# Performance work log

Measured on AMD Instinct MI355X. Metric: run time of the kernel, lower is better.

The kernel has to match this reference:

```python
import jax, jax.numpy as jnp
import numpy as np
from jax import lax

H = 8          # num_heads
STATE = 16     # SSM state_dim
EPS = 1e-5


def layer_norm(x, g, b):
    mu = jnp.mean(x, axis=-1, keepdims=True)
    var = jnp.mean((x - mu) ** 2, axis=-1, keepdims=True)
    return (x - mu) / jnp.sqrt(var + EPS) * g + b


def linear(x, w, b):
    # torch nn.Linear convention: w [out,in]
    return x @ w.T + b


def cross_attn(q_in, kv_in, qw, qb, kw, kb, vw, vb, ow, ob, g, beta):
    B, Lq, D = q_in.shape
    Lk = kv_in.shape[1]
    hd = D // H
    Q = linear(q_in, qw, qb).reshape(B, Lq, H, hd).transpose(0, 2, 1, 3)
    K = linear(kv_in, kw, kb).reshape(B, Lk, H, hd).transpose(0, 2, 1, 3)
    V = linear(kv_in, vw, vb).reshape(B, Lk, H, hd).transpose(0, 2, 1, 3)
    scores = jnp.einsum('bhqd,bhkd->bhqk', Q, K) / (hd ** 0.5)
    w = jax.nn.softmax(scores, axis=-1)
    out = jnp.einsum('bhqk,bhkd->bhqd', w, V)
    out = out.transpose(0, 2, 1, 3).reshape(B, Lq, D)
    out = linear(out, ow, ob)
    out = layer_norm(out + q_in, g, beta)
    return out, w


def ssm(x, in_w, in_b, A, Bm, C, gw, gb, ow, ob):
    B, L, D = x.shape
    xp = linear(x, in_w, in_b)                      # [B,L,2D]
    x_in = xp[..., D:]                              # second chunk
    gate = jax.nn.sigmoid(linear(x, gw, gb))
    x_in = x_in * gate
    def step(h, xt):
        h = h @ A.T + xt @ Bm.T                     # [B,STATE]
        return h, h @ C.T                           # y [B,D]
    h0 = jnp.zeros((B, STATE), dtype=x.dtype)
    _, ys = lax.scan(step, h0, x_in.transpose(1, 0, 2))
    ys = ys.transpose(1, 0, 2)
    return linear(ys, ow, ob)


def mamba_block(x, p, i):
    y = ssm(layer_norm(x, p['m_ln1_g'][i], p['m_ln1_b'][i]),
            p['m_in_w'][i], p['m_in_b'][i], p['m_A'][i], p['m_B'][i], p['m_C'][i],
            p['m_gate_w'][i], p['m_gate_b'][i], p['m_sout_w'][i], p['m_sout_b'][i])
    x = x + y
    h = layer_norm(x, p['m_ln2_g'][i], p['m_ln2_b'][i])
    h = linear(h, p['m_f1_w'][i], p['m_f1_b'][i])
    h = jax.nn.gelu(h, approximate=False)
    h = linear(h, p['m_f2_w'][i], p['m_f2_b'][i])
    return x + h


def setup_inputs() -> dict:
    key = jax.random.key(0)
    ks = iter(jax.random.split(key, 64))
    B, L, D, BD, VD = 1024, 32, 256, 128, 256
    nB = 6
    def rn(shape, s=0.02):
        return jax.random.normal(next(ks), shape, dtype=jnp.float32) * s
    inp = {
        'ble_features': jax.random.normal(next(ks), (B, L, BD), dtype=jnp.float32),
        'visual_features': jax.random.normal(next(ks), (B, L, VD), dtype=jnp.float32),
        # modality projections
        'bp_w': rn((D, BD)), 'bp_b': jnp.zeros(D), 'bp_emb': rn((D,)),
        'bp_g': jnp.ones(D), 'bp_beta': jnp.zeros(D),
        'vp_w': rn((D, VD)), 'vp_b': jnp.zeros(D), 'vp_emb': rn((D,)),
        'vp_g': jnp.ones(D), 'vp_beta': jnp.zeros(D),
        # two cross-attentions stacked on axis 0: [0]=ble->vis, [1]=vis->ble
        'a_qw': rn((2, D, D)), 'a_qb': jnp.zeros((2, D)),
        'a_kw': rn((2, D, D)), 'a_kb': jnp.zeros((2, D)),
        'a_vw': rn((2, D, D)), 'a_vb': jnp.zeros((2, D)),
        'a_ow': rn((2, D, D)), 'a_ob': jnp.zeros((2, D)),
        'a_g': jnp.ones((2, D)), 'a_beta': jnp.zeros((2, D)),
        # 6 mamba blocks stacked on axis 0
        'm_ln1_g': jnp.ones((nB, D)), 'm_ln1_b': jnp.zeros((nB, D)),
        'm_in_w': rn((nB, 2 * D, D)), 'm_in_b': jnp.zeros((nB, 2 * D)),
        'm_A': rn((nB, STATE, STATE)), 'm_B': rn((nB, STATE, D)), 'm_C': rn((nB, D, STATE)),
        'm_gate_w': rn((nB, D, D)), 'm_gate_b': jnp.zeros((nB, D)),
        'm_sout_w': rn((nB, D, D)), 'm_sout_b': jnp.zeros((nB, D)),
        'm_ln2_g': jnp.ones((nB, D)), 'm_ln2_b': jnp.zeros((nB, D)),
        'm_f1_w': rn((nB, 4 * D, D)), 'm_f1_b': jnp.zeros((nB, 4 * D)),
        'm_f2_w': rn((nB, D, 4 * D)), 'm_f2_b': jnp.zeros((nB, D)),
        # final projection
        'fin_g': jnp.ones(D), 'fin_beta': jnp.zeros(D),
        'fin_w': rn((D, D)), 'fin_b': jnp.zeros(D),
    }
    return inp


def reference(ble_features, visual_features,
              bp_w, bp_b, bp_emb, bp_g, bp_beta,
              vp_w, vp_b, vp_emb, vp_g, vp_beta,
              a_qw, a_qb, a_kw, a_kb, a_vw, a_vb, a_ow, a_ob, a_g, a_beta,
              m_ln1_g, m_ln1_b, m_in_w, m_in_b, m_A, m_B, m_C,
              m_gate_w, m_gate_b, m_sout_w, m_sout_b,
              m_ln2_g, m_ln2_b, m_f1_w, m_f1_b, m_f2_w, m_f2_b,
              fin_g, fin_beta, fin_w, fin_b):
    ble = layer_norm(linear(ble_features, bp_w, bp_b) + bp_emb, bp_g, bp_beta)
    vis = layer_norm(linear(visual_features, vp_w, vp_b) + vp_emb, vp_g, vp_beta)
    # seq_len == target_length -> align_sequences is identity
    ble_att, w_b2v = cross_attn(ble, vis, a_qw[0], a_qb[0], a_kw[0], a_kb[0],
                                a_vw[0], a_vb[0], a_ow[0], a_ob[0], a_g[0], a_beta[0])
    vis_att, w_v2b = cross_attn(vis, ble, a_qw[1], a_qb[1], a_kw[1], a_kb[1],
                                a_vw[1], a_vb[1], a_ow[1], a_ob[1], a_g[1], a_beta[1])
    fused = ble_att + vis_att
    p = dict(m_ln1_g=m_ln1_g, m_ln1_b=m_ln1_b, m_in_w=m_in_w, m_in_b=m_in_b,
             m_A=m_A, m_B=m_B, m_C=m_C, m_gate_w=m_gate_w, m_gate_b=m_gate_b,
             m_sout_w=m_sout_w, m_sout_b=m_sout_b, m_ln2_g=m_ln2_g, m_ln2_b=m_ln2_b,
             m_f1_w=m_f1_w, m_f1_b=m_f1_b, m_f2_w=m_f2_w, m_f2_b=m_f2_b)
    for i in range(m_A.shape[0]):
        fused = mamba_block(fused, p, i)
    g = jnp.mean(fused, axis=1)
    g = layer_norm(g, fin_g, fin_beta)
    g = jax.nn.gelu(linear(g, fin_w, fin_b), approximate=False)
    wb = jnp.mean(w_b2v, axis=(1, 2, 3))
    wv = jnp.mean(w_v2b, axis=(1, 2, 3))
    tot = wb + wv + 1e-6
    return (g, wb / tot, wv / tot)
```

## Files before the change

kernel.cpp:

```cpp
#include <hip/hip_runtime.h>
#include <hip/hip_bf16.h>
#include <math.h>

static constexpr int Bsz  = 1024;
static constexpr int Lseq = 32;
static constexpr int Dm   = 256;
static constexpr int NROW = Bsz * Lseq;

typedef __attribute__((ext_vector_type(8))) short bf16x8;
typedef __attribute__((ext_vector_type(4))) float f32x4;

__device__ __forceinline__ float sigm_f(float x) {
    return 1.0f / (1.0f + __expf(-x));
}
__device__ __forceinline__ float gelu_f(float x) {
    const float u = x * (0.7978845608028654f + 0.0356774081f * x * x);
    return x * sigm_f(2.0f * u);
}
__device__ __forceinline__ float b2f(ushort u) {
    union { float f; uint v; } t; t.v = ((uint)u) << 16; return t.f;
}
__device__ __forceinline__ ushort f2b(float f) {
    union { float f; uint v; } t; t.f = f;
    const uint lsb = (t.v >> 16) & 1u;
    t.v += 0x7fffu + lsb;
    return (ushort)(t.v >> 16);
}

#define GLDS(gp, lp) __builtin_amdgcn_global_load_lds( \
    (const __attribute__((address_space(1))) void*)(gp), \
    (__attribute__((address_space(3))) void*)(lp), 16, 0, 0)

template<int ACT, bool OUTBF, int OMAP, int DUAL>
__global__ __launch_bounds__(256)
void mgemm(const ushort* __restrict__ X, const ushort* __restrict__ W,
           const ushort* __restrict__ W2,
           const float* __restrict__ b1, const float* __restrict__ b2,
           float* __restrict__ Cf, ushort* __restrict__ Cb,
           ushort* __restrict__ Cb2, int K, int M)
{
    __shared__ ushort As[4096];
    __shared__ ushort Bs[4096];
    __shared__ ushort Bs2[DUAL ? 4096 : 8];
    __shared__ ushort Rx[DUAL ? 4096 : 8192];
    const int tid = threadIdx.x;
    const int w = tid >> 6, l = tid & 63;

    int f = blockIdx.y * gridDim.x + blockIdx.x;
    const int nwg = gridDim.x * gridDim.y;
    if ((nwg & 7) == 0) f = (f & 7) * (nwg >> 3) + (f >> 3);
    const int n0 = (f / gridDim.x) << 7;
    const int m0 = (f % gridDim.x) << 7;

    const int ric  = l >> 2;
    const int slot = l & 3;
    const int rL0 = (w << 4) + ric;
    const int rL1 = rL0 + 64;
    const int sw0 = slot ^ ((rL0 >> 1) & 3);
    const int sw1 = slot ^ ((rL1 >> 1) & 3);
    const ushort* gA0 = X + (size_t)(n0 + rL0) * K + (sw0 << 3);
    const ushort* gA1 = X + (size_t)(n0 + rL1) * K + (sw1 << 3);
    const ushort* gB0 = W + (size_t)(m0 + rL0) * K + (sw0 << 3);
    const ushort* gB1 = W + (size_t)(m0 + rL1) * K + (sw1 << 3);
    const ushort* gC0 = nullptr; const ushort* gC1 = nullptr;
    if constexpr (DUAL) {
        gC0 = W2 + (size_t)(m0 + rL0) * K + (sw0 << 3);
        gC1 = W2 + (size_t)(m0 + rL1) * K + (sw1 << 3);
    }
    ushort* lA0 = As + ((size_t)w << 9);
    ushort* lA1 = As + ((size_t)(w + 4) << 9);
    ushort* lB0 = Bs + ((size_t)w << 9);
    ushort* lB1 = Bs + ((size_t)(w + 4) << 9);
    ushort* lC0 = Bs2 + ((size_t)w << 9);
    ushort* lC1 = Bs2 + ((size_t)(w + 4) << 9);

    const int wr = (w >> 1) & 1, wc = w & 1;
    const int cl = l & 15, kg = l >> 4;
    int aoff[4], boff[4];
    #pragma unroll
    for (int m = 0; m < 4; ++m) {
        const int r = wr * 64 + m * 16 + cl;
        aoff[m] = r * 32 + ((kg ^ ((r >> 1) & 3)) << 3);
    }
    #pragma unroll
    for (int n = 0; n < 4; ++n) {
        const int r = wc * 64 + n * 16 + cl;
        boff[n] = r * 32 + ((kg ^ ((r >> 1) & 3)) << 3);
    }

    f32x4 acc[4][4];
    f32x4 acc2[DUAL ? 4 : 1][DUAL ? 4 : 1];
    #pragma unroll
    for (int m = 0; m < 4; ++m)
        #pragma unroll
        for (int n = 0; n < 4; ++n) {
            acc[m][n] = (f32x4){0.f, 0.f, 0.f, 0.f};
            if constexpr (DUAL) acc2[m][n] = (f32x4){0.f, 0.f, 0.f, 0.f};
        }

    for (int kc = 0; kc < K; kc += 32) {
        GLDS(gA0, lA0); GLDS(gA1, lA1);
        GLDS(gB0, lB0); GLDS(gB1, lB1);
        gA0 += 32; gA1 += 32; gB0 += 32; gB1 += 32;
        if constexpr (DUAL) {
            GLDS(gC0, lC0); GLDS(gC1, lC1);
            gC0 += 32; gC1 += 32;
        }
        __syncthreads();
        bf16x8 av[4], bv[4];
        #pragma unroll
        for (int m = 0; m < 4; ++m) av[m] = *(const bf16x8*)(As + aoff[m]);
        #pragma unroll
        for (int n = 0; n < 4; ++n) bv[n] = *(const bf16x8*)(Bs + boff[n]);
        #pragma unroll
        for (int m = 0; m < 4; ++m)
            #pragma unroll
            for (int n = 0; n < 4; ++n)
                acc[m][n] = __builtin_amdgcn_mfma_f32_16x16x32_bf16(
                    av[m], bv[n], acc[m][n], 0, 0, 0);
        if constexpr (DUAL) {
            bf16x8 cv[4];
            #pragma unroll
            for (int n = 0; n < 4; ++n) cv[n] = *(const bf16x8*)(Bs2 + boff[n]);
            #pragma unroll
            for (int m = 0; m < 4; ++m)
                #pragma unroll
                for (int n = 0; n < 4; ++n)
                    acc2[m][n] = __builtin_amdgcn_mfma_f32_16x16x32_bf16(
                        av[m], cv[n], acc2[m][n], 0, 0, 0);
        }
        __syncthreads();
    }

    const int colb = m0 + wc * 64 + cl;
    const int rowb = n0 + wr * 64 + (kg << 2);
    float biasA[4], biasB[4];
    #pragma unroll
    for (int n = 0; n < 4; ++n) {
        biasA[n] = (b1 != nullptr) ? b1[colb + n * 16] : 0.0f;
        if constexpr (DUAL) biasB[n] = b2[colb + n * 16];
    }

    if constexpr (OUTBF || DUAL != 0) {
        ushort* Rw;
        if constexpr (DUAL) Rw = (w == 0) ? As : (w == 1) ? Bs : (w == 2) ? Bs2 : Rx;
        else                Rw = (w == 0) ? As : (w == 1) ? Bs : Rx + ((w - 2) << 12);
        const int rr = l >> 3, rc8 = (l & 7) << 3;
        const int nout = (DUAL == 2) ? 2 : 1;
        for (int which = 0; which < nout; ++which) {
            #pragma unroll
            for (int m = 0; m < 4; ++m)
                #pragma unroll
                for (int j = 0; j < 4; ++j) {
                    const int lrow = m * 16 + (kg << 2) + j;
                    #pragma unroll
                    for (int n = 0; n < 4; ++n) {
                        float v;
                        if (which == 0) {
                            v = acc[m][n][j] + biasA[n];
                            if constexpr (DUAL == 1)
                                v = sigm_f(v) * (acc2[m][n][j] + biasB[n]);
                            else if (ACT == 1) v = sigm_f(v);
                            else if (ACT == 2) v = gelu_f(v);
                        } else {
                            v = acc2[m][n][j] + biasB[n];
                        }
                        const int lcol = (n << 4) + cl;
                        Rw[lrow * 64 + (lcol ^ (((lrow >> 1) & 7) << 3))] = f2b(v);
                    }
                }
            ushort* dst = (which == 0) ? Cb : Cb2;
            #pragma unroll
            for (int p = 0; p < 8; ++p) {
                const int lrow = (p << 3) + rr;
                const bf16x8 v8 = *(const bf16x8*)(
                    Rw + lrow * 64 + (rc8 ^ (((lrow >> 1) & 7) << 3)));
                const size_t grow = (size_t)(n0 + wr * 64 + lrow);
                const int gcol = m0 + wc * 64 + rc8;
                size_t idx;
                if (OMAP == 1) idx = grow * 1024 + ((size_t)(gcol >> 4) << 5) + (gcol & 15);
                else           idx = grow * (size_t)M + gcol;
                *(bf16x8*)(dst + idx) = v8;
            }
        }
    } else {
        #pragma unroll
        for (int m = 0; m < 4; ++m)
            #pragma unroll
            for (int j = 0; j < 4; ++j) {
                const size_t row = (size_t)(rowb + m * 16 + j);
                #pragma unroll
                for (int n = 0; n < 4; ++n) {
                    float v = acc[m][n][j] + biasA[n];
                    if (ACT == 1) v = sigm_f(v);
                    else if (ACT == 2) v = gelu_f(v);
                    Cf[row * (size_t)M + colb + n * 16] = v;
                }
            }
    }
}

template<bool ADD_E, bool ACC_F, bool WRV, int LNOUT, bool HASB2>
__global__ __launch_bounds__(256)
void growln_k(const ushort* __restrict__ X, const ushort* __restrict__ W,
              const float* __restrict__ b1, const float* __restrict__ b2,
              const float* __restrict__ E, const float* __restrict__ g,
              const float* __restrict__ bt, float* __restrict__ Fres,
              ushort* __restrict__ Yb, int K)
{
    __shared__ ushort As[64 * 32];
    __shared__ ushort Bs[256 * 32];
    const int tid = threadIdx.x;
    const int w = tid >> 6, l = tid & 63;
    const int n0 = blockIdx.x << 6;

    const int ric = l >> 2, slot = l & 3;
    const int rA  = (w << 4) + ric;
    const int swA = slot ^ ((rA >> 1) & 3);
    const ushort* gA = X + (size_t)(n0 + rA) * K + (swA << 3);
    ushort* lA = As + (w << 9);
    const int rB0 = (w << 4) + ric;
    const int rB1 = rB0 + 64, rB2 = rB0 + 128, rB3 = rB0 + 192;
    const ushort* gB0 = W + (size_t)rB0 * K + ((slot ^ ((rB0 >> 1) & 3)) << 3);
    const ushort* gB1 = W + (size_t)rB1 * K + ((slot ^ ((rB1 >> 1) & 3)) << 3);
    const ushort* gB2 = W + (size_t)rB2 * K + ((slot ^ ((rB2 >> 1) & 3)) << 3);
    const ushort* gB3 = W + (size_t)rB3 * K + ((slot ^ ((rB3 >> 1) & 3)) << 3);
    ushort* lB0 = Bs + (w << 9);
    ushort* lB1 = Bs + ((4 + w) << 9);
    ushort* lB2 = Bs + ((8 + w) << 9);
    ushort* lB3 = Bs + ((12 + w) << 9);

    const int cl = l & 15, kg = l >> 4;
    const int ar = (w << 4) + cl;
    const int aoff = ar * 32 + ((kg ^ ((ar >> 1) & 3)) << 3);
    int boff[16];
    #pragma unroll
    for (int n = 0; n < 16; ++n) {
        const int br = n * 16 + cl;
        boff[n] = br * 32 + ((kg ^ ((br >> 1) & 3)) << 3);
    }

    f32x4 acc[16];
    #pragma unroll
    for (int n = 0; n < 16; ++n) acc[n] = (f32x4){0.f, 0.f, 0.f, 0.f};

    for (int kc = 0; kc < K; kc += 32) {
        GLDS(gA, lA);   gA  += 32;
        GLDS(gB0, lB0); gB0 += 32;
        GLDS(gB1, lB1); gB1 += 32;
        GLDS(gB2, lB2); gB2 += 32;
        GLDS(gB3, lB3); gB3 += 32;
        __syncthreads();
        const bf16x8 av = *(const bf16x8*)(As + aoff);
        #pragma unroll
        for (int n = 0; n < 16; ++n) {
            const bf16x8 bv = *(const bf16x8*)(Bs + boff[n]);
            acc[n] = __builtin_amdgcn_mfma_f32_16x16x32_bf16(av, bv, acc[n], 0, 0, 0);
        }
        __syncthreads();
    }

    float bA[16];
    #pragma unroll
    for (int n = 0; n < 16; ++n) {
        float v = (b1 != nullptr) ? b1[n * 16 + cl] : 0.0f;
        if (HASB2) v += b2[n * 16 + cl];
        bA[n] = v;
    }
    float gg[16], bb[16];
    if (LNOUT > 0) {
        #pragma unroll
        for (int n = 0; n < 16; ++n) { gg[n] = g[n * 16 + cl]; bb[n] = bt[n * 16 + cl]; }
    }

    #pragma unroll
    for (int j = 0; j < 4; ++j) {
        const int r = n0 + (w << 4) + (kg << 2) + j;
        const size_t rb = (size_t)r << 8;
        float v[16];
        float s = 0.0f;
        #pragma unroll
        for (int n = 0; n < 16; ++n) {
            float x = acc[n][j] + bA[n];
            if (ADD_E) x += E[rb + n * 16 + cl];
            if (ACC_F) x += Fres[rb + n * 16 + cl];
            v[n] = x; s += x;
        }
        if (WRV) {
            #pragma unroll
            for (int n = 0; n < 16; ++n) Fres[rb + n * 16 + cl] = v[n];
        }
        if (LNOUT > 0) {
            #pragma unroll
            for (int o = 1; o < 16; o <<= 1) s += __shfl_xor(s, o);
            const float mu = s * (1.0f / 256.0f);
            float q = 0.0f;
            #pragma unroll
            for (int n = 0; n < 16; ++n) { const float d = v[n] - mu; q += d * d; }
            #pragma unroll
            for (int o = 1; o < 16; o <<= 1) q += __shfl_xor(q, o);
            const float rstd = rsqrtf(q * (1.0f / 256.0f) + 1e-5f);
            #pragma unroll
            for (int n = 0; n < 16; ++n) {
                const float y = (v[n] - mu) * rstd * gg[n] + bb[n];
                const size_t idx = rb + n * 16 + cl;
                if (LNOUT & 1) Yb[idx] = f2b(y);
                if (LNOUT == 2 || LNOUT == 3) Fres[idx] = y;
                if (LNOUT == 4) Fres[idx] += y;
            }
        }
    }
}

__global__ __launch_bounds__(256)
void ln_k(const float* __restrict__ X, const float* __restrict__ g,
          const float* __restrict__ bt, ushort* __restrict__ Yb)
{
    const int lane = threadIdx.x & 63;
    const int row  = (blockIdx.x << 2) + (threadIdx.x >> 6);
    const size_t base = (size_t)row * Dm + (lane << 2);
    float4 v = *reinterpret_cast<const float4*>(&X[base]);
    float s = v.x + v.y + v.z + v.w;
    #pragma unroll
    for (int o = 1; o < 64; o <<= 1) s += __shfl_xor(s, o);
    const float mu = s * (1.0f / 256.0f);
    const float d0 = v.x - mu, d1 = v.y - mu, d2 = v.z - mu, d3 = v.w - mu;
    float q = d0*d0 + d1*d1 + d2*d2 + d3*d3;
    #pragma unroll
    for (int o = 1; o < 64; o <<= 1) q += __shfl_xor(q, o);
    const float rstd = rsqrtf(q * (1.0f / 256.0f) + 1e-5f);
    const int c = lane << 2;
    const float4 gg = *reinterpret_cast<const float4*>(&g[c]);
    const float4 bb = *reinterpret_cast<const float4*>(&bt[c]);
    ushort4 ub;
    ub.x = f2b(d0*rstd*gg.x + bb.x); ub.y = f2b(d1*rstd*gg.y + bb.y);
    ub.z = f2b(d2*rstd*gg.z + bb.z); ub.w = f2b(d3*rstd*gg.w + bb.w);
    *reinterpret_cast<ushort4*>(&Yb[base]) = ub;
}

__global__ __launch_bounds__(256)
void attn_k(const ushort* __restrict__ Q, const ushort* __restrict__ K,
            const ushort* __restrict__ V, ushort* __restrict__ O)
{
    __shared__ float Qs[32][33], Ks[32][33], Vs[32][33], Ss[32][33];
    const int bh = blockIdx.x;
    const int b = bh >> 3, h = bh & 7;
    const int tid = threadIdx.x;
    const int r  = tid >> 3;
    const int c4 = (tid & 7) << 2;
    const size_t base = ((size_t)b * Lseq + r) * Dm + h * 32 + c4;
    {
        const ushort4 q = *reinterpret_cast<const ushort4*>(&Q[base]);
        Qs[r][c4+0]=b2f(q.x); Qs[r][c4+1]=b2f(q.y); Qs[r][c4+2]=b2f(q.z); Qs[r][c4+3]=b2f(q.w);
        const ushort4 k = *reinterpret_cast<const ushort4*>(&K[base]);
        Ks[r][c4+0]=b2f(k.x); Ks[r][c4+1]=b2f(k.y); Ks[r][c4+2]=b2f(k.z); Ks[r][c4+3]=b2f(k.w);
        const ushort4 v = *reinterpret_cast<const ushort4*>(&V[base]);
        Vs[r][c4+0]=b2f(v.x); Vs[r][c4+1]=b2f(v.y); Vs[r][c4+2]=b2f(v.z); Vs[r][c4+3]=b2f(v.w);
    }
    __syncthreads();
    float sc[4] = {0.f, 0.f, 0.f, 0.f};
    #pragma unroll
    for (int d = 0; d < 32; ++d) {
        const float qv = Qs[r][d];
        #pragma unroll
        for (int j = 0; j < 4; ++j) sc[j] = fmaf(qv, Ks[c4+j][d], sc[j]);
    }
    #pragma unroll
    for (int j = 0; j < 4; ++j) sc[j] *= 0.17677669529663687f;
    float mx = fmaxf(fmaxf(sc[0], sc[1]), fmaxf(sc[2], sc[3]));
    #pragma unroll
    for (int o = 1; o < 8; o <<= 1) mx = fmaxf(mx, __shfl_xor(mx, o));
    float sum = 0.f;
    #pragma unroll
    for (int j = 0; j < 4; ++j) { sc[j] = __expf(sc[j] - mx); sum += sc[j]; }
    #pragma unroll
    for (int o = 1; o < 8; o <<= 1) sum += __shfl_xor(sum, o);
    const float inv = 1.0f / sum;
    #pragma unroll
    for (int j = 0; j < 4; ++j) Ss[r][c4+j] = sc[j] * inv;
    __syncthreads();
    float o4[4] = {0.f, 0.f, 0.f, 0.f};
    #pragma unroll
    for (int k = 0; k < 32; ++k) {
        const float wv = Ss[r][k];
        #pragma unroll
        for (int j = 0; j < 4; ++j) o4[j] = fmaf(wv, Vs[k][c4+j], o4[j]);
    }
    ushort4 ob; ob.x=f2b(o4[0]); ob.y=f2b(o4[1]); ob.z=f2b(o4[2]); ob.w=f2b(o4[3]);
    *reinterpret_cast<ushort4*>(&O[base]) = ob;
}

__global__ __launch_bounds__(256)
void xb_gemm(const ushort* __restrict__ X, const ushort* __restrict__ Bw,
             ushort* __restrict__ XB)
{
    __shared__ ushort As[128 * 32];
    __shared__ ushort Bsf[16 * 256];
    const int tid = threadIdx.x;
    const int w = tid >> 6, l = tid & 63;
    const int n0 = blockIdx.x << 7;
    #pragma unroll
    for (int rep = 0; rep < 2; ++rep) {
        const int u = (rep << 8) + tid;
        const int r = u >> 5;
        const int c8 = (u & 31) << 3;
        const int di = (r * 256 + c8) ^ ((r & 7) << 3);
        *(bf16x8*)(Bsf + di) = *(const bf16x8*)(Bw + r * 256 + c8);
    }
    const int ric = l >> 2, slot = l & 3;
    const int rL0 = (w << 4) + ric, rL1 = rL0 + 64;
    const int sw0 = slot ^ ((rL0 >> 1) & 3), sw1 = slot ^ ((rL1 >> 1) & 3);
    const ushort* gA0 = X + (size_t)(n0 + rL0) * 256 + (sw0 << 3);
    const ushort* gA1 = X + (size_t)(n0 + rL1) * 256 + (sw1 << 3);
    ushort* lA0 = As + (w << 9);
    ushort* lA1 = As + ((w + 4) << 9);
    const int cl = l & 15, kg = l >> 4;
    int aoff[2];
    #pragma unroll
    for (int m = 0; m < 2; ++m) {
        const int r = w * 32 + m * 16 + cl;
        aoff[m] = r * 32 + ((kg ^ ((r >> 1) & 3)) << 3);
    }
    f32x4 acc[2] = {(f32x4){0.f,0.f,0.f,0.f}, (f32x4){0.f,0.f,0.f,0.f}};
    for (int kc = 0; kc < 256; kc += 32) {
        GLDS(gA0, lA0); GLDS(gA1, lA1);
        gA0 += 32; gA1 += 32;
        __syncthreads();
        const bf16x8 av0 = *(const bf16x8*)(As + aoff[0]);
        const bf16x8 av1 = *(const bf16x8*)(As + aoff[1]);
        const int bidx = (cl * 256 + kc + (kg << 3)) ^ ((cl & 7) << 3);
        const bf16x8 bv = *(const bf16x8*)(Bsf + bidx);
        acc[0] = __builtin_amdgcn_mfma_f32_16x16x32_bf16(av0, bv, acc[0], 0, 0, 0);
        acc[1] = __builtin_amdgcn_mfma_f32_16x16x32_bf16(av1, bv, acc[1], 0, 0, 0);
        __syncthreads();
    }
    #pragma unroll
    for (int m = 0; m < 2; ++m)
        #pragma unroll
        for (int j = 0; j < 4; ++j) {
            const int row = n0 + w * 32 + m * 16 + (kg << 2) + j;
            XB[(size_t)row * 16 + cl] = f2b(acc[m][j]);
        }
}

__global__ __launch_bounds__(256)
void powT_k(const float* __restrict__ A_all, ushort* __restrict__ T_all)
{
    __shared__ float P[2][16][16];
    __shared__ float Asm[16][16];
    const int layer = blockIdx.x;
    const float* A = A_all + layer * 256;
    ushort* T = T_all + (size_t)layer * 262144;
    const int tid = threadIdx.x;
    const int i = tid >> 4, j = tid & 15;
    Asm[i][j] = A[tid];
    const bf16x8 z = {0,0,0,0,0,0,0,0};
    for (int u = tid; u < 32768; u += 256)
        *(bf16x8*)(T + (size_t)u * 8) = z;
    P[0][i][j] = (i == j) ? 1.0f : 0.0f;
    __syncthreads();
    for (int k = 0; k < 32; ++k) {
        const float pv = P[k & 1][i][j];
        const ushort pb = f2b(pv);
        for (int tau = 0; tau + k < 32; ++tau)
            T[(size_t)((tau + k) * 16 + i) * 512 + tau * 16 + j] = pb;
        float acc = 0.0f;
        #pragma unroll
        for (int l2 = 0; l2 < 16; ++l2) acc = fmaf(P[k & 1][i][l2], Asm[l2][j], acc);
        P[(k & 1) ^ 1][i][j] = acc;
        __syncthreads();
    }
}

__global__ __launch_bounds__(256)
void zeroH_k(ushort* __restrict__ Hp)
{
    const int i = blockIdx.x * 256 + threadIdx.x;
    const bf16x8 z = {0,0,0,0,0,0,0,0};
    *(bf16x8*)(Hp + (size_t)i * 8) = z;
}

__global__ __launch_bounds__(256)
void wsc_k(const float* __restrict__ sw, const float* __restrict__ Cc,
           ushort* __restrict__ Wp)
{
    const int i = blockIdx.x >> 4;
    const int m = ((blockIdx.x & 15) << 4) + (threadIdx.x >> 4);
    const int s = threadIdx.x & 15;
    const float* swr = sw + ((size_t)i << 16) + (m << 8);
    const float* cc  = Cc + ((size_t)i << 12) + s;
    float acc = 0.0f;
    #pragma unroll 8
    for (int d = 0; d < 256; ++d) acc = fmaf(swr[d], cc[d << 4], acc);
    ushort* o = Wp + ((size_t)i << 13) + (m << 5);
    o[s] = f2b(acc);
    o[s + 16] = 0;
}

__global__ __launch_bounds__(256)
void meanL_k(const float* __restrict__ X, float* __restrict__ G)
{
    const int idx = blockIdx.x * 256 + threadIdx.x;
    const int b = idx >> 8, d = idx & 255;
    const float* xp = X + (size_t)b * (Lseq * Dm) + d;
    float s = 0.0f;
    #pragma unroll
    for (int t = 0; t < Lseq; ++t) s += xp[t << 8];
    G[idx] = s * (1.0f / 32.0f);
}

__global__ __launch_bounds__(256)
void fillw_k(float* __restrict__ out)
{
    const int i = blockIdx.x * 256 + threadIdx.x;
    const float wm = 1.0f / 32.0f;
    out[i] = wm / (wm + wm + 1e-6f);
}

__global__ __launch_bounds__(256)
void cast_k(const float* __restrict__ src, ushort* __restrict__ dst, int n4)
{
    const int i = blockIdx.x * 256 + threadIdx.x;
    if (i < n4) {
        const float4 v = reinterpret_cast<const float4*>(src)[i];
        ushort4 o; o.x = f2b(v.x); o.y = f2b(v.y); o.z = f2b(v.z); o.w = f2b(v.w);
        reinterpret_cast<ushort4*>(dst)[i] = o;
    }
}

__global__ __launch_bounds__(256)
void cast_inw_k(const float* __restrict__ src, ushort* __restrict__ dst)
{
    const int i = blockIdx.x * 256 + threadIdx.x;
    const int blk = i >> 14, rem = i & 16383;
    const float4 v = reinterpret_cast<const float4*>(
        src + (size_t)blk * 131072 + 65536)[rem];
    ushort4 o; o.x = f2b(v.x); o.y = f2b(v.y); o.z = f2b(v.z); o.w = f2b(v.w);
    reinterpret_cast<ushort4*>(dst)[i] = o;
}

extern "C" void kernel_launch(void* const* d_in, const int* in_sizes, int n_in,
                              void* d_out, int out_size, void* d_ws, size_t ws_size,
                              hipStream_t stream)
{
    const float* ble_f   = (const float*)d_in[0];
    const float* vis_f   = (const float*)d_in[1];
    const float* bp_w    = (const float*)d_in[2];
    const float* bp_b    = (const float*)d_in[3];
    const float* bp_emb  = (const float*)d_in[4];
    const float* bp_g    = (const float*)d_in[5];
    const float* bp_beta = (const float*)d_in[6];
    const float* vp_w    = (const float*)d_in[7];
    const float* vp_b    = (const float*)d_in[8];
    const float* vp_emb  = (const float*)d_in[9];
    const float* vp_g    = (const float*)d_in[10];
    const float* vp_beta = (const float*)d_in[11];
    const float* a_qw    = (const float*)d_in[12];
    const float* a_qb    = (const float*)d_in[13];
    const float* a_kw    = (const float*)d_in[14];
    const float* a_kb    = (const float*)d_in[15];
    const float* a_vw    = (const float*)d_in[16];
    const float* a_vb    = (const float*)d_in[17];
    const float* a_ow    = (const float*)d_in[18];
    const float* a_ob    = (const float*)d_in[19];
    const float* a_g     = (const float*)d_in[20];
    const float* a_beta  = (const float*)d_in[21];
    const float* m_ln1_g = (const float*)d_in[22];
    const float* m_ln1_b = (const float*)d_in[23];
    const float* m_in_w  = (const float*)d_in[24];
    const float* m_in_b  = (const float*)d_in[25];
    const float* m_A     = (const float*)d_in[26];
    const float* m_B     = (const float*)d_in[27];
    const float* m_C     = (const float*)d_in[28];
    const float* m_gw    = (const float*)d_in[29];
    const float* m_gb    = (const float*)d_in[30];
    const float* m_sw    = (const float*)d_in[31];
    const float* m_sb    = (const float*)d_in[32];
    const float* m_ln2_g = (const float*)d_in[33];
    const float* m_ln2_b = (const float*)d_in[34];
    const float* m_f1w   = (const float*)d_in[35];
    const float* m_f1b   = (const float*)d_in[36];
    const float* m_f2w   = (const float*)d_in[37];
    const float* m_f2b   = (const float*)d_in[38];
    const float* fin_g   = (const float*)d_in[39];
    const float* fin_beta= (const float*)d_in[40];
    const float* fin_w   = (const float*)d_in[41];
    const float* fin_b   = (const float*)d_in[42];

    float* out = (float*)d_out;
    float* ws  = (float*)d_ws;
    const size_t NDf = (size_t)NROW * Dm;

    float* F_res = ws;
    float* F0 = ws + 1 * NDf;
    float* F1 = ws + 2 * NDf;
    float* F2 = ws + 3 * NDf;
    ushort* S0 = (ushort*)(ws + 4 * NDf);
    ushort* S1 = S0 + NDf;
    ushort* S2 = S1 + NDf;
    ushort* S3 = S2 + NDf;
    ushort* S4 = S3 + NDf;
    ushort* Wa = S4 + NDf;
    ushort* W_bp  = Wa;
    ushort* W_vp  = W_bp + 32768;
    ushort* W_q   = W_vp + 65536;
    ushort* W_k   = W_q + 131072;
    ushort* W_v   = W_k + 131072;
    ushort* W_o   = W_v + 131072;
    ushort* W_g   = W_o + 131072;
    ushort* W_in  = W_g + 393216;
    ushort* W_f1  = W_in + 393216;
    ushort* W_f2  = W_f1 + 1572864;
    ushort* W_fin = W_f2 + 1572864;
    ushort* W_sc  = W_fin + 65536;
    ushort* Hpad  = W_sc + 49152;
    ushort* B_ble = (ushort*)F2;
    ushort* B_vis = B_ble + (size_t)NROW * 128;
    ushort* T_all = (ushort*)F2;
    ushort* W_bm  = T_all + 1572864;
    ushort* XBuf  = W_bm + 24576;

    const dim3 blk(256);
    auto cgrid = [](int n4) { return dim3((n4 + 255) / 256); };

    cast_k<<<cgrid(1048576), blk, 0, stream>>>(ble_f, B_ble, 1048576);
    cast_k<<<cgrid(2097152), blk, 0, stream>>>(vis_f, B_vis, 2097152);
    cast_k<<<cgrid(8192),   blk, 0, stream>>>(bp_w, W_bp, 8192);
    cast_k<<<cgrid(16384),  blk, 0, stream>>>(vp_w, W_vp, 16384);
    cast_k<<<cgrid(32768),  blk, 0, stream>>>(a_qw, W_q, 32768);
    cast_k<<<cgrid(32768),  blk, 0, stream>>>(a_kw, W_k, 32768);
    cast_k<<<cgrid(32768),  blk, 0, stream>>>(a_vw, W_v, 32768);
    cast_k<<<cgrid(32768),  blk, 0, stream>>>(a_ow, W_o, 32768);
    cast_k<<<cgrid(98304),  blk, 0, stream>>>(m_gw, W_g, 98304);
    cast_k<<<cgrid(393216), blk, 0, stream>>>(m_f1w, W_f1, 393216);
    cast_k<<<cgrid(393216), blk, 0, stream>>>(m_f2w, W_f2, 393216);
    cast_k<<<cgrid(16384),  blk, 0, stream>>>(fin_w, W_fin, 16384);
    cast_inw_k<<<cgrid(98304), blk, 0, stream>>>(m_in_w, W_in);
    wsc_k<<<96, blk, 0, stream>>>(m_sw, m_C, W_sc);

    auto gg = [](int M, int N) { return dim3(M / 128, N / 128); };
    const dim3 gRow(NROW / 64);

    growln_k<false,false,false,3,true><<<gRow, blk, 0, stream>>>(
        B_ble, W_bp, bp_b, bp_emb, nullptr, bp_g, bp_beta, F0, S0, 128);
    growln_k<false,false,false,3,true><<<gRow, blk, 0, stream>>>(
        B_vis, W_vp, vp_b, vp_emb, nullptr, vp_g, vp_beta, F1, S1, 256);

    for (int a = 0; a < 2; ++a) {
        const ushort* qin_b = (a == 0) ? S0 : S1;
        const ushort* kin_b = (a == 0) ? S1 : S0;
        const float*  qin_f = (a == 0) ? F0 : F1;
        const size_t wo = (size_t)a * 65536;
        const size_t bo = (size_t)a * 256;
        mgemm<0,true,0,0><<<gg(256, NROW), blk, 0, stream>>>(
            qin_b, W_q + wo, nullptr, a_qb + bo, nullptr, nullptr, S4, nullptr, 256, 256);
        mgemm<0,true,0,2><<<gg(256, NROW), blk, 0, stream>>>(
            kin_b, W_k + wo, W_v + wo, a_kb + bo, a_vb + bo, nullptr, S2, S3, 256, 256);
        attn_k<<<Bsz * 8, blk, 0, stream>>>(S4, S2, S3, S4);
        if (a == 0)
            growln_k<true,false,false,2,false><<<gRow, blk, 0, stream>>>(
                S4, W_o + wo, a_ob + bo, nullptr, qin_f, a_g + bo, a_beta + bo, F_res, nullptr, 256);
        else
            growln_k<true,false,false,4,false><<<gRow, blk, 0, stream>>>(
                S4, W_o + wo, a_ob + bo, nullptr, qin_f, a_g + bo, a_beta + bo, F_res, nullptr, 256);
    }

    powT_k<<<6, blk, 0, stream>>>(m_A, T_all);
    cast_k<<<cgrid(6144), blk, 0, stream>>>(m_B, W_bm, 6144);
    zeroH_k<<<512, blk, 0, stream>>>(Hpad);

    ln_k<<<NROW/4, blk, 0, stream>>>(F_res, m_ln1_g, m_ln1_b, S0);

    for (int i = 0; i < 6; ++i) {
        mgemm<0,true,0,1><<<gg(256, NROW), blk, 0, stream>>>(
            S0, W_g + (size_t)i*65536, W_in + (size_t)i*65536,
            m_gb + i*256, m_in_b + (size_t)i*512 + 256, nullptr, S2, nullptr, 256, 256);
        xb_gemm<<<NROW/128, blk, 0, stream>>>(S2, W_bm + (size_t)i*4096, XBuf);
        mgemm<0,true,1,0><<<gg(512, 1024), blk, 0, stream>>>(
            XBuf, T_all + (size_t)i*262144, nullptr, nullptr, nullptr, nullptr, Hpad, nullptr, 512, 512);
        growln_k<false,true,true,1,false><<<gRow, blk, 0, stream>>>(
            Hpad, W_sc + (size_t)i*8192, m_sb + i*256, nullptr, nullptr,
            m_ln2_g + i*256, m_ln2_b + i*256, F_res, S0, 32);
        mgemm<2,true,0,0><<<gg(1024, NROW), blk, 0, stream>>>(
            S0, W_f1 + (size_t)i*262144, nullptr, m_f1b + i*1024, nullptr, nullptr, S1, nullptr, 256, 1024);
        if (i < 5)
            growln_k<false,true,true,1,false><<<gRow, blk, 0, stream>>>(
                S1, W_f2 + (size_t)i*262144, m_f2b + i*256, nullptr, nullptr,
                m_ln1_g + (i+1)*256, m_ln1_b + (i+1)*256, F_res, S0, 1024);
        else
            growln_k<false,true,true,0,false><<<gRow, blk, 0, stream>>>(
                S1, W_f2 + (size_t)i*262144, m_f2b + i*256, nullptr, nullptr,
                nullptr, nullptr, F_res, nullptr, 1024);
    }

    meanL_k<<<(Bsz * Dm) / 256, blk, 0, stream>>>(F_res, F0);
    ln_k<<<Bsz/4, blk, 0, stream>>>(F0, fin_g, fin_beta, S1);
    mgemm<2,false,0,0><<<gg(256, Bsz), blk, 0, stream>>>(
        S1, W_fin, nullptr, fin_b, nullptr, out, nullptr, nullptr, 256, 256);
    fillw_k<<<8, blk, 0, stream>>>(out + (size_t)Bsz * Dm);
}
```

Measured before the change: 1.306 ms.

## Split growln row tile across 2x2 warp grid with shared-memory LayerNorm reduction

The fused GEMM+LayerNorm kernel now handles 32 rows per block instead of 64. The four waves form a 2x2 grid, each covering 16 rows by 128 columns, so accumulators drop from 16 to 8 MFMA tiles per wave. Row mean and variance partials from the two column halves are combined through shared memory with extra barriers. The aim is to cut register pressure and double the block count for better occupancy and load balance. The cost is reloading the full W tile for every 32 rows, which doubles weight traffic, plus two extra syncs.

After: 1.293 ms. No clear change (-1.0%).

```diff
diff --git a/kernel.cpp b/kernel.cpp
--- a/kernel.cpp
+++ b/kernel.cpp
@@ -208,102 +208,123 @@
               const float* __restrict__ bt, float* __restrict__ Fres,
               ushort* __restrict__ Yb, int K)
 {
-    __shared__ ushort As[64 * 32];
+    __shared__ ushort As[32 * 32];
     __shared__ ushort Bs[256 * 32];
+    __shared__ float sred[32][2];
+    __shared__ float qred[32][2];
     const int tid = threadIdx.x;
     const int w = tid >> 6, l = tid & 63;
-    const int n0 = blockIdx.x << 6;
+    const int n0 = blockIdx.x << 5;
+    const int rowg = w >> 1, colg = w & 1;
 
     const int ric = l >> 2, slot = l & 3;
-    const int rA  = (w << 4) + ric;
-    const int swA = slot ^ ((rA >> 1) & 3);
-    const ushort* gA = X + (size_t)(n0 + rA) * K + (swA << 3);
-    ushort* lA = As + (w << 9);
-    const int rB0 = (w << 4) + ric;
-    const int rB1 = rB0 + 64, rB2 = rB0 + 128, rB3 = rB0 + 192;
-    const ushort* gB0 = W + (size_t)rB0 * K + ((slot ^ ((rB0 >> 1) & 3)) << 3);
-    const ushort* gB1 = W + (size_t)rB1 * K + ((slot ^ ((rB1 >> 1) & 3)) << 3);
-    const ushort* gB2 = W + (size_t)rB2 * K + ((slot ^ ((rB2 >> 1) & 3)) << 3);
-    const ushort* gB3 = W + (size_t)rB3 * K + ((slot ^ ((rB3 >> 1) & 3)) << 3);
-    ushort* lB0 = Bs + (w << 9);
-    ushort* lB1 = Bs + ((4 + w) << 9);
-    ushort* lB2 = Bs + ((8 + w) << 9);
-    ushort* lB3 = Bs + ((12 + w) << 9);
+    const ushort* gB[4]; ushort* lB[4];
+    #pragma unroll
+    for (int c = 0; c < 4; ++c) {
+        const int rB = ((w << 2) + c) * 16 + ric;
+        gB[c] = W + (size_t)rB * K + ((slot ^ ((rB >> 1) & 3)) << 3);
+        lB[c] = Bs + (((w << 2) + c) << 9);
+    }
+    const ushort* gA = nullptr; ushort* lA = nullptr;
+    if (w < 2) {
+        const int rA = (w << 4) + ric;
+        gA = X + (size_t)(n0 + rA) * K + ((slot ^ ((rA >> 1) & 3)) << 3);
+        lA = As + (w << 9);
+    }
 
     const int cl = l & 15, kg = l >> 4;
-    const int ar = (w << 4) + cl;
+    const int ar = rowg * 16 + cl;
     const int aoff = ar * 32 + ((kg ^ ((ar >> 1) & 3)) << 3);
-    int boff[16];
-    #pragma unroll
-    for (int n = 0; n < 16; ++n) {
-        const int br = n * 16 + cl;
+    int boff[8];
+    #pragma unroll
+    for (int n = 0; n < 8; ++n) {
+        const int br = colg * 128 + n * 16 + cl;
         boff[n] = br * 32 + ((kg ^ ((br >> 1) & 3)) << 3);
     }
 
-    f32x4 acc[16];
-    #pragma unroll
-    for (int n = 0; n < 16; ++n) acc[n] = (f32x4){0.f, 0.f, 0.f, 0.f};
+    f32x4 acc[8];
+    #pragma unroll
+    for (int n = 0; n < 8; ++n) acc[n] = (f32x4){0.f, 0.f, 0.f, 0.f};
 
     for (int kc = 0; kc < K; kc += 32) {
-        GLDS(gA, lA);   gA  += 32;
-        GLDS(gB0, lB0); gB0 += 32;
-        GLDS(gB1, lB1); gB1 += 32;
-        GLDS(gB2, lB2); gB2 += 32;
-        GLDS(gB3, lB3); gB3 += 32;
+        #pragma unroll
+        for (int c = 0; c < 4; ++c) { GLDS(gB[c], lB[c]); gB[c] += 32; }
+        if (w < 2) { GLDS(gA, lA); gA += 32; }
         __syncthreads();
         const bf16x8 av = *(const bf16x8*)(As + aoff);
         #pragma unroll
-        for (int n = 0; n < 16; ++n) {
+        for (int n = 0; n < 8; ++n) {
             const bf16x8 bv = *(const bf16x8*)(Bs + boff[n]);
             acc[n] = __builtin_amdgcn_mfma_f32_16x16x32_bf16(av, bv, acc[n], 0, 0, 0);
         }
         __syncthreads();
     }
 
-    float bA[16];
-    #pragma unroll
-    for (int n = 0; n < 16; ++n) {
-        float v = (b1 != nullptr) ? b1[n * 16 + cl] : 0.0f;
-        if (HASB2) v += b2[n * 16 + cl];
+    float bA[8];
+    #pragma unroll
+    for (int n = 0; n < 8; ++n) {
+        const int col = colg * 128 + n * 16 + cl;
+        float v = (b1 != nullptr) ? b1[col] : 0.0f;
+        if (HASB2) v += b2[col];
         bA[n] = v;
     }
-    float gg[16], bb[16];
+    float gg[8], bb[8];
     if (LNOUT > 0) {
         #pragma unroll
-        for (int n = 0; n < 16; ++n) { gg[n] = g[n * 16 + cl]; bb[n] = bt[n * 16 + cl]; }
+        for (int n = 0; n < 8; ++n) {
+            const int col = colg * 128 + n * 16 + cl;
+            gg[n] = g[col]; bb[n] = bt[col];
+        }
     }
 
     #pragma unroll
     for (int j = 0; j < 4; ++j) {
-        const int r = n0 + (w << 4) + (kg << 2) + j;
-        const size_t rb = (size_t)r << 8;
-        float v[16];
+        const int lrow = rowg * 16 + (kg << 2) + j;
+        const size_t rb = (size_t)(n0 + lrow) << 8;
         float s = 0.0f;
         #pragma unroll
-        for (int n = 0; n < 16; ++n) {
+        for (int n = 0; n < 8; ++n) {
+            const size_t idx = rb + colg * 128 + n * 16 + cl;
             float x = acc[n][j] + bA[n];
-            if (ADD_E) x += E[rb + n * 16 + cl];
-            if (ACC_F) x += Fres[rb + n * 16 + cl];
-            v[n] = x; s += x;
+            if (ADD_E) x += E[idx];
+            if (ACC_F) x += Fres[idx];
+            acc[n][j] = x; s += x;
         }
         if (WRV) {
             #pragma unroll
-            for (int n = 0; n < 16; ++n) Fres[rb + n * 16 + cl] = v[n];
+            for (int n = 0; n < 8; ++n)
+                Fres[rb + colg * 128 + n * 16 + cl] = acc[n][j];
         }
         if (LNOUT > 0) {
             #pragma unroll
             for (int o = 1; o < 16; o <<= 1) s += __shfl_xor(s, o);
-            const float mu = s * (1.0f / 256.0f);
+            if (cl == 0) sred[lrow][colg] = s;
+        }
+    }
+    if (LNOUT > 0) {
+        __syncthreads();
+        float mu[4];
+        #pragma unroll
+        for (int j = 0; j < 4; ++j) {
+            const int lrow = rowg * 16 + (kg << 2) + j;
+            mu[j] = (sred[lrow][0] + sred[lrow][1]) * (1.0f / 256.0f);
             float q = 0.0f;
             #pragma unroll
-            for (int n = 0; n < 16; ++n) { const float d = v[n] - mu; q += d * d; }
+            for (int n = 0; n < 8; ++n) { const float d = acc[n][j] - mu[j]; q += d * d; }
             #pragma unroll
             for (int o = 1; o < 16; o <<= 1) q += __shfl_xor(q, o);
-            const float rstd = rsqrtf(q * (1.0f / 256.0f) + 1e-5f);
-            #pragma unroll
-            for (int n = 0; n < 16; ++n) {
-                const float y = (v[n] - mu) * rstd * gg[n] + bb[n];
-                const size_t idx = rb + n * 16 + cl;
+            if (cl == 0) qred[lrow][colg] = q;
+        }
+        __syncthreads();
+        #pragma unroll
+        for (int j = 0; j < 4; ++j) {
+            const int lrow = rowg * 16 + (kg << 2) + j;
+            const size_t rb = (size_t)(n0 + lrow) << 8;
+            const float rstd = rsqrtf((qred[lrow][0] + qred[lrow][1]) * (1.0f / 256.0f) + 1e-5f);
+            #pragma unroll
+            for (int n = 0; n < 8; ++n) {
+                const float y = (acc[n][j] - mu[j]) * rstd * gg[n] + bb[n];
+                const size_t idx = rb + colg * 128 + n * 16 + cl;
                 if (LNOUT & 1) Yb[idx] = f2b(y);
                 if (LNOUT == 2 || LNOUT == 3) Fres[idx] = y;
                 if (LNOUT == 4) Fres[idx] += y;
@@ -639,7 +660,7 @@
     wsc_k<<<96, blk, 0, stream>>>(m_sw, m_C, W_sc);
 
     auto gg = [](int M, int N) { return dim3(M / 128, N / 128); };
-    const dim3 gRow(NROW / 64);
+    const dim3 gRow(NROW / 32);
 
     growln_k<false,false,false,3,true><<<gRow, blk, 0, stream>>>(
         B_ble, W_bp, bp_b, bp_emb, nullptr, bp_g, bp_beta, F0, S0, 128);
```
